# Optimization experiments

Measured on AMD Instinct MI355X. Metric: run time of the kernel, lower is better.

## Reference

```python
import jax, jax.numpy as jnp
import numpy as np
from jax import lax

L, D, H, V = 4, 128, 4, 33
d = D // H  # 32
B, T = 32, 4096

def rms(x, w, eps=1e-5):
    ms = jnp.mean(x.astype(jnp.float32) ** 2, axis=-1, keepdims=True)
    return (x * lax.rsqrt(ms + eps).astype(x.dtype)) * w

def l2n(x, eps=1e-6):
    return x * lax.rsqrt(jnp.sum(x * x, axis=-1, keepdims=True) + eps)

def causal_conv(h, w, b):
    # h: [B,T,D], w: [D,1,K] depthwise, b: [D]; causal via left-pad K-1
    K = w.shape[-1]
    y = lax.conv_general_dilated(h.transpose(0, 2, 1), w, (1,), [(K - 1, 0)],
                                 feature_group_count=h.shape[-1],
                                 dimension_numbers=('NCH', 'OIH', 'NCH'))
    return y.transpose(0, 2, 1) + b

def delta_scan(q, k, v, beta):
    # q,k,v: [B,T,H,d]; beta: [B,T,H]. Rank-1 delta-rule recurrence over T.
    xs = tuple(jnp.moveaxis(a, 1, 0) for a in (q, k, v, beta))
    S0 = jnp.zeros((q.shape[0], q.shape[2], q.shape[3], q.shape[3]), q.dtype)
    def step(S, inp):
        qt, kt, vt, bt = inp
        err = (vt - jnp.einsum('bhij,bhi->bhj', S, kt)) * bt[..., None]
        S = S + kt[..., :, None] * err[..., None, :]
        return S, jnp.einsum('bhij,bhi->bhj', S, qt)
    _, o = lax.scan(step, S0, xs)
    return jnp.moveaxis(o, 0, 1)  # [B,T,H,d]

def setup_inputs() -> dict:
    key = jax.random.key(0)
    ks = iter(jax.random.split(key, 40))
    def rn(shape, scale=0.02):
        return jax.random.normal(next(ks), shape, jnp.float32) * scale
    return {
        'x': jax.random.randint(next(ks), (B, T), 0, V),
        'emb': rn((V, D)),
        'qw': rn((L, D, D)), 'kw': rn((L, D, D)), 'vw': rn((L, D, D)),
        'qcw': rn((L, D, 1, 4), 0.2), 'qcb': rn((L, D)),
        'kcw': rn((L, D, 1, 4), 0.2), 'kcb': rn((L, D)),
        'vcw': rn((L, D, 1, 4), 0.2), 'vcb': rn((L, D)),
        'ow': rn((L, D, D)), 'gw': rn((L, D, D)), 'bw': rn((L, H, D)),
        'hnw': jnp.ones((L, d), jnp.float32),
        'n1w': jnp.ones((L, D), jnp.float32), 'n2w': jnp.ones((L, D), jnp.float32),
        'm1w': rn((L, 2 * D, D)), 'm2w': rn((L, D, 2 * D)),
        'fnw': jnp.ones((D,), jnp.float32), 'hw': rn((V, D)),
    }

def reference(x, emb, qw, kw, vw, qcw, qcb, kcw, kcb, vcw, vcb, ow, gw, bw,
              hnw, n1w, n2w, m1w, m2w, fnw, hw):
    silu = jax.nn.silu
    h = emb[x]  # [B,T,D]
    for l in range(L):
        hn = rms(h, n1w[l])
        q = l2n(silu(causal_conv(hn @ qw[l].T, qcw[l], qcb[l])).reshape(B, T, H, d)) / jnp.sqrt(jnp.float32(d))
        k = l2n(silu(causal_conv(hn @ kw[l].T, kcw[l], kcb[l])).reshape(B, T, H, d))
        v = silu(causal_conv(hn @ vw[l].T, vcw[l], vcb[l])).reshape(B, T, H, d)
        gate = (hn @ gw[l].T).reshape(B, T, H, d)
        beta = jax.nn.sigmoid(hn @ bw[l].T)  # [B,T,H]
        o = delta_scan(q, k, v, beta)
        o = rms(o, hnw[l]) * silu(gate)
        h = h + o.reshape(B, T, D) @ ow[l].T
        h = h + silu(rms(h, n2w[l]) @ m1w[l].T) @ m2w[l].T
    return rms(h, fnw) @ hw.T  # [B,T,V]
```

## Files before the change

kernel.cpp:

```cpp
#include <hip/hip_runtime.h>
#include <hip/hip_bf16.h>
#include <math.h>

#define BB 32
#define TT 4096
#define DD 128
#define HH 4
#define dh 32
#define VV 33
#define LL 4
#define MM (BB*TT)
#define NCHUNK (MM/128)
#define NC 64

typedef short short8 __attribute__((ext_vector_type(8)));
typedef float f32x4 __attribute__((ext_vector_type(4)));

__device__ __forceinline__ float b2f(unsigned short u){
  union{float f; unsigned int x;} v; v.x = ((unsigned int)u)<<16; return v.f;
}
__device__ __forceinline__ unsigned short f2b(float f){
  union{float f; unsigned int x;} v; v.f=f;
  unsigned int r = v.x + 0x7fffu + ((v.x>>16)&1u);
  return (unsigned short)(r>>16);
}
__device__ __forceinline__ float blo(unsigned int u){ union{float f;unsigned int x;}v; v.x=u<<16; return v.f;}
__device__ __forceinline__ float bhi(unsigned int u){ union{float f;unsigned int x;}v; v.x=u&0xffff0000u; return v.f;}
__device__ __forceinline__ float siluf(float x){ return x/(1.0f+expf(-x)); }

__global__ __launch_bounds__(256) void k_embed(const int* __restrict__ x, const float* __restrict__ emb,
                                               float* __restrict__ h){
  int i = blockIdx.x*256 + threadIdx.x;
  int bt = i>>7, c = i&127;
  h[i] = emb[x[bt]*DD + c];
}

__global__ __launch_bounds__(256) void k_rms(const float* __restrict__ src, const float* __restrict__ w,
                                             unsigned short* __restrict__ dst){
  int row = blockIdx.x*4 + (threadIdx.x>>6);
  int lane = threadIdx.x&63;
  const float2 xv = *(const float2*)(src + (size_t)row*DD + lane*2);
  float ss = xv.x*xv.x + xv.y*xv.y;
  #pragma unroll
  for (int m=1;m<64;m<<=1) ss += __shfl_xor(ss,m,64);
  float sc = rsqrtf(ss*(1.0f/128.0f)+1e-5f);
  const float2 wv = *(const float2*)(w + lane*2);
  unsigned int o = ((unsigned int)f2b(xv.y*sc*wv.y)<<16) | (unsigned int)f2b(xv.x*sc*wv.x);
  *(unsigned int*)(dst + (size_t)row*DD + lane*2) = o;
}

template<int NP, int ACT, int OUTADD>
__global__ __launch_bounds__(256) void k_gemm(const unsigned short* __restrict__ A,
                                              const float* __restrict__ W,
                                              void* __restrict__ outp, int N, int K){
  __shared__ __align__(16) unsigned short As[128*128];
  __shared__ __align__(16) unsigned short Ws[64*128];
  const int tid = threadIdx.x;
  const int lane = tid & 63, wave = tid >> 6;
  const int row0 = blockIdx.x*128, colbase = blockIdx.y*(64*NP);
  const int wr0 = (wave&1)*64, wc0 = (wave>>1)*32;
  const int fr = lane & 15, fq = lane >> 4;
  f32x4 acc[NP][4][2];
  #pragma unroll
  for (int p=0;p<NP;p++)
    #pragma unroll
    for (int m=0;m<4;m++)
      #pragma unroll
      for (int n=0;n<2;n++) acc[p][m][n] = (f32x4){0.f,0.f,0.f,0.f};

  for (int kc=0; kc<K; kc+=128){
    #pragma unroll
    for (int ii=0; ii<8; ++ii){
      int flat = tid + ii*256;
      int r = flat>>4, g = flat&15;
      uint4 gv = *(const uint4*)(A + (size_t)(row0+r)*K + kc + g*8);
      *(uint4*)&As[r*128 + ((g^(r&7))<<3)] = gv;
    }
    #pragma unroll
    for (int p=0;p<NP;p++){
      const int col0 = colbase + p*64;
      #pragma unroll
      for (int ii=0; ii<8; ++ii){
        int flat = tid + ii*256;
        int n = flat>>5, q4 = flat&31;
        float4 wv = *(const float4*)(W + (size_t)(col0+n)*K + kc + q4*4);
        uint2 pk;
        pk.x = (unsigned int)f2b(wv.x) | ((unsigned int)f2b(wv.y)<<16);
        pk.y = (unsigned int)f2b(wv.z) | ((unsigned int)f2b(wv.w)<<16);
        int dst = n*128 + ((((q4>>1)^(n&7))<<3) | ((q4&1)<<2));
        *(uint2*)&Ws[dst] = pk;
      }
      __syncthreads();
      #pragma unroll
      for (int ks=0; ks<4; ++ks){
        int gg = ks*4 + fq;
        short8 a[4], b[2];
        #pragma unroll
        for (int m=0;m<4;m++){
          int row = wr0 + m*16 + fr;
          a[m] = *(const short8*)&As[row*128 + ((gg^(row&7))<<3)];
        }
        #pragma unroll
        for (int n=0;n<2;n++){
          int col = wc0 + n*16 + fr;
          b[n] = *(const short8*)&Ws[col*128 + ((gg^(col&7))<<3)];
        }
        #pragma unroll
        for (int m=0;m<4;m++){
          #pragma unroll
          for (int n=0;n<2;n++)
            acc[p][m][n] = __builtin_amdgcn_mfma_f32_16x16x32_bf16(a[m], b[n], acc[p][m][n], 0, 0, 0);
        }
      }
      __syncthreads();
    }
  }

  #pragma unroll
  for (int p=0;p<NP;p++){
    const int col0 = colbase + p*64;
    if (OUTADD){
      float* O = (float*)outp;
      #pragma unroll
      for (int m=0;m<4;m++){
        #pragma unroll
        for (int n=0;n<2;n++){
          int ccol = col0 + wc0 + n*16 + fr;
          #pragma unroll
          for (int r=0;r<4;r++){
            int rrow = row0 + wr0 + m*16 + fq*4 + r;
            O[(size_t)rrow*N + ccol] += acc[p][m][n][r];
          }
        }
      }
    } else {
      unsigned short* O = (unsigned short*)outp;
      #pragma unroll
      for (int m=0;m<4;m++){
        #pragma unroll
        for (int n=0;n<2;n++){
          int ccol = col0 + wc0 + n*16 + fr;
          #pragma unroll
          for (int r=0;r<4;r++){
            int rrow = row0 + wr0 + m*16 + fq*4 + r;
            float vv = acc[p][m][n][r];
            if (ACT) vv = siluf(vv);
            O[(size_t)rrow*N + ccol] = f2b(vv);
          }
        }
      }
    }
  }
}

__global__ __launch_bounds__(256) void k_headm(const unsigned short* __restrict__ A,
                                               const float* __restrict__ W,
                                               float* __restrict__ out){
  __shared__ __align__(16) unsigned short As[128*128];
  __shared__ __align__(16) unsigned short Ws[64*128];
  const int tid = threadIdx.x;
  const int lane = tid & 63, wave = tid >> 6;
  const int row0 = blockIdx.x*128;
  const int wr0 = (wave&1)*64, wc0 = (wave>>1)*32;
  const int fr = lane & 15, fq = lane >> 4;
  f32x4 acc[4][2];
  #pragma unroll
  for (int m=0;m<4;m++)
    #pragma unroll
    for (int n=0;n<2;n++) acc[m][n] = (f32x4){0.f,0.f,0.f,0.f};

  #pragma unroll
  for (int ii=0; ii<8; ++ii){
    int flat = tid + ii*256;
    int r = flat>>4, g = flat&15;
    uint4 gv = *(const uint4*)(A + (size_t)(row0+r)*DD + g*8);
    *(uint4*)&As[r*128 + ((g^(r&7))<<3)] = gv;
  }
  #pragma unroll
  for (int ii=0; ii<8; ++ii){
    int flat = tid + ii*256;
    int n = flat>>5, q4 = flat&31;
    float4 wv = (n < VV) ? *(const float4*)(W + (size_t)n*DD + q4*4)
                         : (float4){0.f,0.f,0.f,0.f};
    uint2 pk;
    pk.x = (unsigned int)f2b(wv.x) | ((unsigned int)f2b(wv.y)<<16);
    pk.y = (unsigned int)f2b(wv.z) | ((unsigned int)f2b(wv.w)<<16);
    int dst = n*128 + ((((q4>>1)^(n&7))<<3) | ((q4&1)<<2));
    *(uint2*)&Ws[dst] = pk;
  }
  __syncthreads();
  #pragma unroll
  for (int ks=0; ks<4; ++ks){
    int gg = ks*4 + fq;
    short8 a[4], b[2];
    #pragma unroll
    for (int m=0;m<4;m++){
      int row = wr0 + m*16 + fr;
      a[m] = *(const short8*)&As[row*128 + ((gg^(row&7))<<3)];
    }
    #pragma unroll
    for (int n=0;n<2;n++){
      int col = wc0 + n*16 + fr;
      b[n] = *(const short8*)&Ws[col*128 + ((gg^(col&7))<<3)];
    }
    #pragma unroll
    for (int m=0;m<4;m++){
      #pragma unroll
      for (int n=0;n<2;n++)
        acc[m][n] = __builtin_amdgcn_mfma_f32_16x16x32_bf16(a[m], b[n], acc[m][n], 0, 0, 0);
    }
  }
  #pragma unroll
  for (int m=0;m<4;m++){
    #pragma unroll
    for (int n=0;n<2;n++){
      int ccol = wc0 + n*16 + fr;
      if (ccol < VV){
        #pragma unroll
        for (int r=0;r<4;r++){
          int rrow = row0 + wr0 + m*16 + fq*4 + r;
          out[(size_t)rrow*VV + ccol] = acc[m][n][r];
        }
      }
    }
  }
}

__global__ __launch_bounds__(256) void k_beta(const unsigned short* __restrict__ hn,
                                              const float* __restrict__ bwl, float* __restrict__ beta){
  __shared__ unsigned short As[64*128];
  int tid = threadIdx.x; int row0 = blockIdx.x*64;
  #pragma unroll
  for (int ii=0;ii<4;ii++){
    int flat = tid + ii*256;
    int r = flat>>4, v16 = flat&15;
    *(uint4*)&As[r*128 + v16*8] = *(const uint4*)(hn + (size_t)(row0+r)*DD + v16*8);
  }
  __syncthreads();
  int r = tid>>2, n = tid&3;
  const float* wr = bwl + n*DD;
  const unsigned short* ar = &As[r*128];
  float s = 0.f;
  #pragma unroll
  for (int k=0;k<128;k+=8){
    uint4 a = *(const uint4*)(ar + k);
    float4 wa = *(const float4*)(wr + k);
    float4 wb = *(const float4*)(wr + k + 4);
    s += blo(a.x)*wa.x + bhi(a.x)*wa.y + blo(a.y)*wa.z + bhi(a.y)*wa.w;
    s += blo(a.z)*wb.x + bhi(a.z)*wb.y + blo(a.w)*wb.z + bhi(a.w)*wb.w;
  }
  beta[(size_t)(row0+r)*HH + n] = 1.0f/(1.0f+expf(-s));
}

__global__ __launch_bounds__(256) void k_halo(const unsigned short* __restrict__ A,
                                              const unsigned short* __restrict__ B,
                                              const unsigned short* __restrict__ C,
                                              unsigned short* __restrict__ halo){
  int i = blockIdx.x*256 + threadIdx.x;
  int ch = i & 127;
  int rt = i >> 7;
  int r3 = rt % 3;
  int tn = (rt/3) % 3;
  int ck = rt / 9;
  unsigned short v = 0;
  if ((ck & 31) != 0){
    const unsigned short* X = (tn==0) ? A : (tn==1) ? B : C;
    v = X[((size_t)ck*128 - 3 + r3)*DD + ch];
  }
  halo[(size_t)i] = v;
}

__global__ __launch_bounds__(256) void k_conv_ip(
    unsigned short* __restrict__ A, unsigned short* __restrict__ B, unsigned short* __restrict__ C,
    const float* __restrict__ qcw, const float* __restrict__ qcb,
    const float* __restrict__ kcw, const float* __restrict__ kcb,
    const float* __restrict__ vcw, const float* __restrict__ vcb,
    const unsigned short* __restrict__ halo){
  __shared__ __align__(16) unsigned short Xs[131*128];
  const int tid = threadIdx.x;
  const int ck = blockIdx.x, tn = blockIdx.y;
  unsigned short* X = (tn==0) ? A : (tn==1) ? B : C;
  const float* w = (tn==0) ? qcw : (tn==1) ? kcw : vcw;
  const float* bi = (tn==0) ? qcb : (tn==1) ? kcb : vcb;

  if (tid < 48){
    int lr = tid>>4, c16 = tid&15;
    *(uint4*)&Xs[lr*128 + c16*8] = *(const uint4*)&halo[((size_t)(ck*3+tn)*3 + lr)*128 + c16*8];
  }
  #pragma unroll
  for (int ii=0; ii<8; ++ii){
    int flat = tid + ii*256;
    int r = flat>>4, c16 = flat&15;
    *(uint4*)&Xs[(3+r)*128 + c16*8] = *(const uint4*)&X[((size_t)ck*128 + r)*DD + c16*8];
  }
  __syncthreads();

  const int rh = tid>>7, c = tid&127;
  float w0=w[c*4+0], w1=w[c*4+1], w2=w[c*4+2], w3=w[c*4+3];
  float bc = bi[c];
  #pragma unroll 2
  for (int rr=0; rr<64; ++rr){
    int row = rr*2 + rh;
    float y = bc + w0*b2f(Xs[(row+0)*128+c]) + w1*b2f(Xs[(row+1)*128+c])
                 + w2*b2f(Xs[(row+2)*128+c]) + w3*b2f(Xs[(row+3)*128+c]);
    y = siluf(y);
    if (tn < 2){
      float s = y*y;
      #pragma unroll
      for (int m=1;m<32;m<<=1) s += __shfl_xor(s,m,64);
      y *= rsqrtf(s + 1e-6f);
      if (tn==0) y *= 0.17677669529663687f;
    }
    X[((size_t)ck*128 + row)*DD + c] = f2b(y);
  }
}

__global__ __launch_bounds__(256) void k_pA(const unsigned short* __restrict__ kbuf,
                                            unsigned short* vwbuf,
                                            const float* __restrict__ betab,
                                            unsigned short* __restrict__ Ubuf){
  __shared__ float Abt[64][68];
  __shared__ float sol[64][72];
  __shared__ float bs[64];
  const int c = blockIdx.x, bh = blockIdx.y;
  const int b = bh>>2, h = bh&3;
  const int tid = threadIdx.x;
  const int wave = tid>>6, lane = tid&63;
  const int fr = lane&15, fg = lane>>4;
  const size_t base = ((size_t)b*TT + c*64)*128 + h*32;
  const size_t bbase = ((size_t)b*TT + c*64)*4 + h;
  const size_t ub = ((size_t)bh*NC + c)*2048;

  if (tid < 64) bs[tid] = betab[bbase + (size_t)tid*4];

  short8 kA  = *(const short8*)(kbuf + base + (size_t)(wave*16+fr)*128 + fg*8);
  short8 kB0 = *(const short8*)(kbuf + base + (size_t)( 0+fr)*128 + fg*8);
  short8 kB1 = *(const short8*)(kbuf + base + (size_t)(16+fr)*128 + fg*8);
  short8 kB2 = *(const short8*)(kbuf + base + (size_t)(32+fr)*128 + fg*8);
  short8 kB3 = *(const short8*)(kbuf + base + (size_t)(48+fr)*128 + fg*8);
  __syncthreads();

  {
    float4 bsv = *(const float4*)&bs[wave*16 + fg*4];
    f32x4 a;
    #define BUILD(nt, kB) if (wave >= nt){ \
      a = (f32x4){0.f,0.f,0.f,0.f}; \
      a = __builtin_amdgcn_mfma_f32_16x16x32_bf16(kA, kB, a, 0,0,0); \
      Abt[nt*16+fr][wave*16+fg*4+0] = a[0]*bsv.x; \
      Abt[nt*16+fr][wave*16+fg*4+1] = a[1]*bsv.y; \
      Abt[nt*16+fr][wave*16+fg*4+2] = a[2]*bsv.z; \
      Abt[nt*16+fr][wave*16+fg*4+3] = a[3]*bsv.w; }
    BUILD(0, kB0) BUILD(1, kB1) BUILD(2, kB2) BUILD(3, kB3)
    #undef BUILD
  }

  const unsigned short* xp = ((lane<32)? (const unsigned short*)vwbuf : kbuf) + base + (lane&31);
  float racc[16];
  #pragma unroll
  for (int r=0;r<16;r++)
    racc[r] = b2f(xp[(size_t)(wave*16+r)*128]) * bs[wave*16+r];

  #pragma unroll
  for (int p=0;p<4;p++){
    if (wave == p){
      #pragma unroll
      for (int r=0;r<16;r++){
        float w_ = racc[r];
        sol[p*16+r][lane] = w_;
        #pragma unroll
        for (int r2=r+1;r2<16;r2++)
          racc[r2] -= Abt[p*16+r][p*16+r2] * w_;
      }
    }
    __syncthreads();
    if (wave > p){
      #pragma unroll
      for (int s16=0;s16<16;s16++){
        float w_ = sol[p*16+s16][lane];
        #pragma unroll
        for (int r=0;r<16;r++)
          racc[r] -= Abt[p*16+s16][wave*16+r] * w_;
      }
    }
    __syncthreads();
  }

  {
    int row = tid>>2, qt = tid&3;
    if (qt < 2){
      #pragma unroll
      for (int i=0;i<8;i++){
        int col = qt*16 + i*2;
        unsigned int pk = (unsigned int)f2b(sol[row][col]) | ((unsigned int)f2b(sol[row][col+1])<<16);
        *(unsigned int*)(vwbuf + base + (size_t)row*128 + col) = pk;
      }
    } else {
      #pragma unroll
      for (int i=0;i<8;i++){
        int col = (qt-2)*16 + i*2;
        unsigned int pk = (unsigned int)f2b(sol[row][32+col]) | ((unsigned int)f2b(sol[row][33+col])<<16);
        *(unsigned int*)(Ubuf + ub + row*32 + col) = pk;
      }
    }
  }
}

template<int PREC>
__global__ __launch_bounds__(64) void k_pB(const unsigned short* __restrict__ kbuf,
                                           unsigned short* webuf,
                                           const unsigned short* __restrict__ Ubuf,
                                           void* __restrict__ SentP){
  __shared__ float Sl[32][33];
  __shared__ unsigned short El[64][40];
  __shared__ unsigned short Ell[64][40];
  __shared__ unsigned short Kl[64][40];
  const int bh = blockIdx.x, b = bh>>2, h = bh&3;
  const int lane = threadIdx.x, fr = lane&15, fg = lane>>4;
  for (int i=lane; i<32*33; i+=64) ((float*)Sl)[i] = 0.f;
  f32x4 sc[2][2];
  #pragma unroll
  for (int it=0;it<2;it++){
    #pragma unroll
    for (int ct=0;ct<2;ct++) sc[it][ct]=(f32x4){0.f,0.f,0.f,0.f};
  }

  for (int c=0;c<NC;c++){
    const size_t base = ((size_t)b*TT + c*64)*128 + h*32;
    const size_t ub = ((size_t)bh*NC + c)*2048;
    {
      const unsigned short* kr = kbuf + base + (size_t)lane*128;
      const unsigned short* wr = webuf + base + (size_t)lane*128;
      uint4 a0=*(const uint4*)(kr),   a1=*(const uint4*)(kr+8);
      uint4 a2=*(const uint4*)(kr+16),a3=*(const uint4*)(kr+24);
      uint4 b0=*(const uint4*)(wr),   b1=*(const uint4*)(wr+8);
      uint4 b2=*(const uint4*)(wr+16),b3=*(const uint4*)(wr+24);
      *(uint4*)&Kl[lane][0]=a0; *(uint4*)&Kl[lane][8]=a1;
      *(uint4*)&Kl[lane][16]=a2; *(uint4*)&Kl[lane][24]=a3;
      *(uint4*)&El[lane][0]=b0; *(uint4*)&El[lane][8]=b1;
      *(uint4*)&El[lane][16]=b2; *(uint4*)&El[lane][24]=b3;
    }
    short8 uf[4];
    #pragma unroll
    for (int mt=0;mt<4;mt++)
      uf[mt] = *(const short8*)(Ubuf + ub + (size_t)(mt*16+fr)*32 + fg*8);
    f32x4 acc[4][2];
    #pragma unroll
    for (int mt=0;mt<4;mt++){
      #pragma unroll
      for (int ct=0;ct<2;ct++){
        #pragma unroll
        for (int r=0;r<4;r++)
          acc[mt][ct][r] = b2f(El[mt*16+fg*4+r][ct*16+fr]);
      }
    }
    short8 sb[2], sbl[2];
    #pragma unroll
    for (int ct=0;ct<2;ct++){
      short8 neg, negl;
      float pos[8];
      #pragma unroll
      for (int jj=0;jj<8;jj++){
        float sv = Sl[fg*8+jj][ct*16+fr];
        pos[jj] = sv;
        float nv = -sv;
        unsigned short hi = f2b(nv);
        neg[jj]=(short)hi;
        negl[jj]=(short)f2b(nv - b2f(hi));
      }
      sb[ct]=neg; sbl[ct]=negl;
      if (PREC){
        float* Sf = (float*)SentP + ((size_t)bh*NC + c)*1024 + ct*512 + lane*8;
        *(float4*)Sf     = (float4){pos[0],pos[1],pos[2],pos[3]};
        *(float4*)(Sf+4) = (float4){pos[4],pos[5],pos[6],pos[7]};
      } else {
        short8 p8;
        #pragma unroll
        for (int jj=0;jj<8;jj++) p8[jj]=(short)f2b(pos[jj]);
        *(short8*)((unsigned short*)SentP + ((size_t)bh*NC + c)*1024 + ct*512 + lane*8) = p8;
      }
    }
    #pragma unroll
    for (int mt=0;mt<4;mt++){
      #pragma unroll
      for (int ct=0;ct<2;ct++){
        acc[mt][ct] = __builtin_amdgcn_mfma_f32_16x16x32_bf16(uf[mt], sb[ct],  acc[mt][ct],0,0,0);
        acc[mt][ct] = __builtin_amdgcn_mfma_f32_16x16x32_bf16(uf[mt], sbl[ct], acc[mt][ct],0,0,0);
      }
    }
    #pragma unroll
    for (int mt=0;mt<4;mt++){
      #pragma unroll
      for (int ct=0;ct<2;ct++){
        #pragma unroll
        for (int r=0;r<4;r++){
          float ef = acc[mt][ct][r];
          unsigned short eh = f2b(ef);
          int t = mt*16+fg*4+r, j = ct*16+fr;
          El[t][j] = eh;
          Ell[t][j] = f2b(ef - b2f(eh));
          webuf[base + (size_t)t*128 + j] = eh;
        }
      }
    }
    short8 ka[2][2], eb[2][2], ebl[2][2];
    #pragma unroll
    for (int it=0;it<2;it++){
      #pragma unroll
      for (int ks=0;ks<2;ks++){
        short8 tmp;
        #pragma unroll
        for (int jj=0;jj<8;jj++) tmp[jj] = (short)Kl[ks*32+fg*8+jj][it*16+fr];
        ka[it][ks]=tmp;
      }
    }
    #pragma unroll
    for (int ct=0;ct<2;ct++){
      #pragma unroll
      for (int ks=0;ks<2;ks++){
        short8 t1v, t2v;
        #pragma unroll
        for (int jj=0;jj<8;jj++){
          t1v[jj] = (short)El[ks*32+fg*8+jj][ct*16+fr];
          t2v[jj] = (short)Ell[ks*32+fg*8+jj][ct*16+fr];
        }
        eb[ct][ks]=t1v; ebl[ct][ks]=t2v;
      }
    }
    #pragma unroll
    for (int it=0;it<2;it++){
      #pragma unroll
      for (int ct=0;ct<2;ct++){
        #pragma unroll
        for (int ks=0;ks<2;ks++){
          sc[it][ct] = __builtin_amdgcn_mfma_f32_16x16x32_bf16(ka[it][ks], eb[ct][ks],  sc[it][ct],0,0,0);
          sc[it][ct] = __builtin_amdgcn_mfma_f32_16x16x32_bf16(ka[it][ks], ebl[ct][ks], sc[it][ct],0,0,0);
        }
      }
    }
    #pragma unroll
    for (int it=0;it<2;it++){
      #pragma unroll
      for (int ct=0;ct<2;ct++){
        #pragma unroll
        for (int r=0;r<4;r++)
          Sl[it*16+fg*4+r][ct*16+fr] = sc[it][ct][r];
      }
    }
  }
}

template<int PREC>
__global__ __launch_bounds__(64) void k_pC(unsigned short* qobuf,
                                           const unsigned short* __restrict__ kbuf,
                                           const unsigned short* __restrict__ ebuf,
                                           const void* __restrict__ SentP){
  __shared__ unsigned short Pl[64][72];
  __shared__ unsigned short Plo[64][72];
  __shared__ unsigned short El[64][40];
  const int c = blockIdx.x, bh = blockIdx.y, b=bh>>2, h=bh&3;
  const int lane=threadIdx.x, fr=lane&15, fg=lane>>4;
  const size_t base = ((size_t)b*TT + c*64)*128 + h*32;
  #pragma unroll
  for (int i=0;i<9;i++){
    *(uint4*)&Pl[lane][i*8]  = (uint4){0u,0u,0u,0u};
    *(uint4*)&Plo[lane][i*8] = (uint4){0u,0u,0u,0u};
  }
  {
    const unsigned short* er = ebuf + base + (size_t)lane*128;
    uint4 a0=*(const uint4*)(er),   a1=*(const uint4*)(er+8);
    uint4 a2=*(const uint4*)(er+16),a3=*(const uint4*)(er+24);
    *(uint4*)&El[lane][0]=a0; *(uint4*)&El[lane][8]=a1;
    *(uint4*)&El[lane][16]=a2; *(uint4*)&El[lane][24]=a3;
  }
  short8 qf[4], kf[4];
  #pragma unroll
  for (int mt=0;mt<4;mt++){
    qf[mt] = *(const short8*)(qobuf + base + (size_t)(mt*16+fr)*128 + fg*8);
    kf[mt] = *(const short8*)(kbuf  + base + (size_t)(mt*16+fr)*128 + fg*8);
  }
  #pragma unroll
  for (int mt=0;mt<4;mt++){
    #pragma unroll
    for (int nt=0;nt<4;nt++){
      if (nt>mt) continue;
      f32x4 p = (f32x4){0.f,0.f,0.f,0.f};
      p = __builtin_amdgcn_mfma_f32_16x16x32_bf16(qf[mt], kf[nt], p,0,0,0);
      #pragma unroll
      for (int r=0;r<4;r++){
        int t = mt*16+fg*4+r, s = nt*16+fr;
        float pv = p[r];
        unsigned short ph = f2b(pv);
        Pl[t][s]  = (s<=t)? ph : (unsigned short)0;
        Plo[t][s] = (s<=t)? f2b(pv - b2f(ph)) : (unsigned short)0;
      }
    }
  }
  f32x4 acc[4][2];
  #pragma unroll
  for (int mt=0;mt<4;mt++){
    #pragma unroll
    for (int ct=0;ct<2;ct++) acc[mt][ct]=(f32x4){0.f,0.f,0.f,0.f};
  }
  if (PREC){
    short8 sfh[2], sfl[2];
    #pragma unroll
    for (int ct=0;ct<2;ct++){
      const float* Sf = (const float*)SentP + ((size_t)bh*NC + c)*1024 + ct*512 + lane*8;
      float4 v0 = *(const float4*)Sf;
      float4 v1 = *(const float4*)(Sf+4);
      float sv[8] = {v0.x,v0.y,v0.z,v0.w,v1.x,v1.y,v1.z,v1.w};
      short8 hh, ll;
      #pragma unroll
      for (int jj=0;jj<8;jj++){
        unsigned short hi = f2b(sv[jj]);
        hh[jj]=(short)hi; ll[jj]=(short)f2b(sv[jj]-b2f(hi));
      }
      sfh[ct]=hh; sfl[ct]=ll;
    }
    #pragma unroll
    for (int mt=0;mt<4;mt++){
      #pragma unroll
      for (int ct=0;ct<2;ct++){
        acc[mt][ct]=__builtin_amdgcn_mfma_f32_16x16x32_bf16(qf[mt], sfh[ct], acc[mt][ct],0,0,0);
        acc[mt][ct]=__builtin_amdgcn_mfma_f32_16x16x32_bf16(qf[mt], sfl[ct], acc[mt][ct],0,0,0);
      }
    }
  } else {
    short8 sf[2];
    #pragma unroll
    for (int ct=0;ct<2;ct++)
      sf[ct] = *(const short8*)((const unsigned short*)SentP + ((size_t)bh*NC + c)*1024 + ct*512 + lane*8);
    #pragma unroll
    for (int mt=0;mt<4;mt++){
      #pragma unroll
      for (int ct=0;ct<2;ct++)
        acc[mt][ct]=__builtin_amdgcn_mfma_f32_16x16x32_bf16(qf[mt], sf[ct], acc[mt][ct],0,0,0);
    }
  }
  short8 ebf[2][2];
  #pragma unroll
  for (int ct=0;ct<2;ct++){
    #pragma unroll
    for (int ks=0;ks<2;ks++){
      short8 tmp;
      #pragma unroll
      for (int jj=0;jj<8;jj++) tmp[jj]=(short)El[ks*32+fg*8+jj][ct*16+fr];
      ebf[ct][ks]=tmp;
    }
  }
  #pragma unroll
  for (int mt=0;mt<4;mt++){
    #pragma unroll
    for (int ks=0;ks<2;ks++){
      short8 pa  = *(const short8*)&Pl[mt*16+fr][ks*32+fg*8];
      short8 pal = *(const short8*)&Plo[mt*16+fr][ks*32+fg*8];
      #pragma unroll
      for (int ct=0;ct<2;ct++){
        acc[mt][ct]=__builtin_amdgcn_mfma_f32_16x16x32_bf16(pa,  ebf[ct][ks], acc[mt][ct],0,0,0);
        acc[mt][ct]=__builtin_amdgcn_mfma_f32_16x16x32_bf16(pal, ebf[ct][ks], acc[mt][ct],0,0,0);
      }
    }
  }
  #pragma unroll
  for (int mt=0;mt<4;mt++){
    #pragma unroll
    for (int ct=0;ct<2;ct++){
      #pragma unroll
      for (int r=0;r<4;r++)
        qobuf[base + (size_t)(mt*16+fg*4+r)*128 + ct*16+fr] = f2b(acc[mt][ct][r]);
    }
  }
}

__global__ __launch_bounds__(64) void k_scan(const unsigned short* q, const unsigned short* k,
                                             const unsigned short* v, const float* beta,
                                             unsigned short* o){
  int b = blockIdx.x>>2, hh = blockIdx.x&3;
  int lane = threadIdx.x;
  int j = lane&31, ih = lane>>5;
  float S[16];
  #pragma unroll
  for (int m=0;m<16;m++) S[m]=0.f;
  size_t idx0 = ((size_t)b*TT*HH + hh)*dh;
  size_t bidx0 = (size_t)b*TT*HH + hh;
  const unsigned short* kp = k + idx0 + ih*16;
  const unsigned short* qp = q + idx0 + ih*16;
  for (int t=0;t<TT;t++){
    size_t ofs=(size_t)t*128;
    uint4 ka=*(const uint4*)(kp+ofs), kb=*(const uint4*)(kp+ofs+8);
    uint4 qa=*(const uint4*)(qp+ofs), qb=*(const uint4*)(qp+ofs+8);
    float kf[16], qf[16];
    kf[0]=blo(ka.x);kf[1]=bhi(ka.x);kf[2]=blo(ka.y);kf[3]=bhi(ka.y);
    kf[4]=blo(ka.z);kf[5]=bhi(ka.z);kf[6]=blo(ka.w);kf[7]=bhi(ka.w);
    kf[8]=blo(kb.x);kf[9]=bhi(kb.x);kf[10]=blo(kb.y);kf[11]=bhi(kb.y);
    kf[12]=blo(kb.z);kf[13]=bhi(kb.z);kf[14]=blo(kb.w);kf[15]=bhi(kb.w);
    qf[0]=blo(qa.x);qf[1]=bhi(qa.x);qf[2]=blo(qa.y);qf[3]=bhi(qa.y);
    qf[4]=blo(qa.z);qf[5]=bhi(qa.z);qf[6]=blo(qa.w);qf[7]=bhi(qa.w);
    qf[8]=blo(qb.x);qf[9]=bhi(qb.x);qf[10]=blo(qb.y);qf[11]=bhi(qb.y);
    qf[12]=blo(qb.z);qf[13]=bhi(qb.z);qf[14]=blo(qb.w);qf[15]=bhi(qb.w);
    float vc = b2f(v[idx0+ofs+j]), bc = beta[bidx0+(size_t)t*4];
    float p0=0,p1=0,p2=0,p3=0;
    #pragma unroll
    for (int m=0;m<4;m++){
      p0 += S[m]*kf[m]; p1 += S[m+4]*kf[m+4]; p2 += S[m+8]*kf[m+8]; p3 += S[m+12]*kf[m+12];
    }
    float p = (p0+p1)+(p2+p3);
    p += __shfl_xor(p, 32, 64);
    float err = (vc - p)*bc;
    float o0=0,o1=0,o2=0,o3=0;
    #pragma unroll
    for (int m=0;m<4;m++){
      S[m]    += kf[m]*err;     o0 += S[m]*qf[m];
      S[m+4]  += kf[m+4]*err;   o1 += S[m+4]*qf[m+4];
      S[m+8]  += kf[m+8]*err;   o2 += S[m+8]*qf[m+8];
      S[m+12] += kf[m+12]*err;  o3 += S[m+12]*qf[m+12];
    }
    float oo = (o0+o1)+(o2+o3);
    oo += __shfl_xor(oo, 32, 64);
    if (ih==0) o[idx0 + ofs + j] = f2b(oo);
  }
}

__global__ __launch_bounds__(256) void k_ogate(const unsigned short* __restrict__ o, const unsigned short* __restrict__ gate,
                                               const float* __restrict__ hnwl, unsigned short* __restrict__ tmp){
  int tid=threadIdx.x;
  size_t bt = (size_t)blockIdx.x*2 + (tid>>7);
  int c = tid&127;
  size_t i = bt*DD + c;
  float ov = b2f(o[i]);
  float ss = ov*ov;
  #pragma unroll
  for (int m=1;m<32;m<<=1) ss += __shfl_xor(ss,m,64);
  float r = rsqrtf(ss*(1.0f/32.0f)+1e-5f);
  float g = b2f(gate[i]);
  tmp[i] = f2b(ov*r*hnwl[c&31]*siluf(g));
}

extern "C" void kernel_launch(void* const* d_in, const int* in_sizes, int n_in,
                              void* d_out, int out_size, void* d_ws, size_t ws_size,
                              hipStream_t stream){
  const int*   x   = (const int*)d_in[0];
  const float* emb = (const float*)d_in[1];
  const float* qw  = (const float*)d_in[2];
  const float* kw  = (const float*)d_in[3];
  const float* vw  = (const float*)d_in[4];
  const float* qcw = (const float*)d_in[5];
  const float* qcb = (const float*)d_in[6];
  const float* kcw = (const float*)d_in[7];
  const float* kcb = (const float*)d_in[8];
  const float* vcw = (const float*)d_in[9];
  const float* vcb = (const float*)d_in[10];
  const float* ow  = (const float*)d_in[11];
  const float* gw  = (const float*)d_in[12];
  const float* bw  = (const float*)d_in[13];
  const float* hnw = (const float*)d_in[14];
  const float* n1w = (const float*)d_in[15];
  const float* n2w = (const float*)d_in[16];
  const float* m1w = (const float*)d_in[17];
  const float* m2w = (const float*)d_in[18];
  const float* fnw = (const float*)d_in[19];
  const float* hw  = (const float*)d_in[20];

  char* ws = (char*)d_ws;
  size_t off = 0;
  float* h             = (float*)(ws+off);          off += (size_t)MM*DD*4;
  unsigned short* hn   = (unsigned short*)(ws+off); off += (size_t)MM*DD*2;
  unsigned short* A    = (unsigned short*)(ws+off); off += (size_t)MM*DD*2;
  unsigned short* B    = (unsigned short*)(ws+off); off += (size_t)MM*DD*2;
  unsigned short* C    = (unsigned short*)(ws+off); off += (size_t)MM*DD*2;
  float* beta          = (float*)(ws+off);          off += (size_t)MM*HH*4;
  unsigned short* halo = (unsigned short*)(ws+off); off += (size_t)NCHUNK*9*128*2;
  unsigned short* U    = (unsigned short*)(ws+off); off += (size_t)MM*DD*2;
  void* SentP          = (void*)(ws+off);
  const size_t NEED1 = off + (size_t)8192*1024*4;
  const size_t NEED0 = off + (size_t)8192*1024*2;
  unsigned short* t1   = A;
  const int mode = (ws_size >= NEED1) ? 1 : (ws_size >= NEED0) ? 0 : -1;

  k_embed<<<MM*DD/256, 256, 0, stream>>>(x, emb, h);
  for (int l=0;l<LL;l++){
    k_rms<<<MM/4,256,0,stream>>>(h, n1w + l*DD, hn);
    k_gemm<2,0,0><<<dim3(MM/128,1),256,0,stream>>>(hn, qw + l*DD*DD, A, 128, 128);
    k_gemm<2,0,0><<<dim3(MM/128,1),256,0,stream>>>(hn, kw + l*DD*DD, B, 128, 128);
    k_gemm<2,0,0><<<dim3(MM/128,1),256,0,stream>>>(hn, vw + l*DD*DD, C, 128, 128);
    k_beta<<<MM/64,256,0,stream>>>(hn, bw + l*HH*DD, beta);
    k_halo<<<NCHUNK*9*128/256,256,0,stream>>>(A, B, C, halo);
    k_conv_ip<<<dim3(NCHUNK,3),256,0,stream>>>(A, B, C,
                                  qcw+l*DD*4, qcb+l*DD, kcw+l*DD*4, kcb+l*DD, vcw+l*DD*4, vcb+l*DD,
                                  halo);
    if (mode >= 0){
      k_pA<<<dim3(NC, BB*HH), 256, 0, stream>>>(B, C, beta, U);
      if (mode==1){
        k_pB<1><<<BB*HH, 64, 0, stream>>>(B, C, U, SentP);
        k_pC<1><<<dim3(NC, BB*HH), 64, 0, stream>>>(A, B, C, SentP);
      } else {
        k_pB<0><<<BB*HH, 64, 0, stream>>>(B, C, U, SentP);
        k_pC<0><<<dim3(NC, BB*HH), 64, 0, stream>>>(A, B, C, SentP);
      }
    } else {
      k_scan<<<BB*HH,64,0,stream>>>(A, B, C, beta, A);
    }
    k_gemm<2,0,0><<<dim3(MM/128,1),256,0,stream>>>(hn, gw + l*DD*DD, C, 128, 128);
    k_ogate<<<MM/2,256,0,stream>>>(A, C, hnw+l*dh, B);
    k_gemm<2,0,1><<<dim3(MM/128,1),256,0,stream>>>(B, ow + l*DD*DD, h, 128, 128);
    k_rms<<<MM/4,256,0,stream>>>(h, n2w + l*DD, hn);
    k_gemm<2,1,0><<<dim3(MM/128,2),256,0,stream>>>(hn, m1w + l*2*DD*DD, t1, 256, 128);
    k_gemm<2,0,1><<<dim3(MM/128,1),256,0,stream>>>(t1, m2w + l*2*DD*DD, h, 128, 256);
  }
  k_rms<<<MM/4,256,0,stream>>>(h, fnw, hn);
  k_headm<<<MM/128,256,0,stream>>>(hn, hw, (float*)d_out);
}
```

Before: 2.831 ms.

## Fuse Q/K/V projections into one kernel and parallelize chunk-state scan over 4 waves

```diff
diff --git a/kernel.cpp b/kernel.cpp
--- a/kernel.cpp
+++ b/kernel.cpp
@@ -146,6 +146,88 @@
             float vv = acc[p][m][n][r];
             if (ACT) vv = siluf(vv);
             O[(size_t)rrow*N + ccol] = f2b(vv);
+          }
+        }
+      }
+    }
+  }
+}
+
+__global__ __launch_bounds__(256) void k_qkv(const unsigned short* __restrict__ Ain,
+                                             const float* __restrict__ qw,
+                                             const float* __restrict__ kw,
+                                             const float* __restrict__ vw,
+                                             unsigned short* __restrict__ Oq,
+                                             unsigned short* __restrict__ Ok,
+                                             unsigned short* __restrict__ Ov){
+  __shared__ __align__(16) unsigned short As[128*128];
+  __shared__ __align__(16) unsigned short Ws[64*128];
+  const int tid = threadIdx.x;
+  const int lane = tid & 63, wave = tid >> 6;
+  const int row0 = blockIdx.x*128;
+  const int wr0 = (wave&1)*64, wc0 = (wave>>1)*32;
+  const int fr = lane & 15, fq = lane >> 4;
+
+  #pragma unroll
+  for (int ii=0; ii<8; ++ii){
+    int flat = tid + ii*256;
+    int r = flat>>4, g = flat&15;
+    uint4 gv = *(const uint4*)(Ain + (size_t)(row0+r)*DD + g*8);
+    *(uint4*)&As[r*128 + ((g^(r&7))<<3)] = gv;
+  }
+  for (int t=0;t<3;t++){
+    const float* W = (t==0)?qw:(t==1)?kw:vw;
+    unsigned short* O = (t==0)?Oq:(t==1)?Ok:Ov;
+    for (int p=0;p<2;p++){
+      const int col0 = p*64;
+      #pragma unroll
+      for (int ii=0; ii<8; ++ii){
+        int flat = tid + ii*256;
+        int n = flat>>5, q4 = flat&31;
+        float4 wv = *(const float4*)(W + (size_t)(col0+n)*DD + q4*4);
+        uint2 pk;
+        pk.x = (unsigned int)f2b(wv.x) | ((unsigned int)f2b(wv.y)<<16);
+        pk.y = (unsigned int)f2b(wv.z) | ((unsigned int)f2b(wv.w)<<16);
+        int dst = n*128 + ((((q4>>1)^(n&7))<<3) | ((q4&1)<<2));
+        *(uint2*)&Ws[dst] = pk;
+      }
+      __syncthreads();
+      f32x4 acc[4][2];
+      #pragma unroll
+      for (int m=0;m<4;m++)
+        #pragma unroll
+        for (int n=0;n<2;n++) acc[m][n] = (f32x4){0.f,0.f,0.f,0.f};
+      #pragma unroll
+      for (int ks=0; ks<4; ++ks){
+        int gg = ks*4 + fq;
+        short8 a[4], b[2];
+        #pragma unroll
+        for (int m=0;m<4;m++){
+          int row = wr0 + m*16 + fr;
+          a[m] = *(const short8*)&As[row*128 + ((gg^(row&7))<<3)];
+        }
+        #pragma unroll
+        for (int n=0;n<2;n++){
+          int col = wc0 + n*16 + fr;
+          b[n] = *(const short8*)&Ws[col*128 + ((gg^(col&7))<<3)];
+        }
+        #pragma unroll
+        for (int m=0;m<4;m++){
+          #pragma unroll
+          for (int n=0;n<2;n++)
+            acc[m][n] = __builtin_amdgcn_mfma_f32_16x16x32_bf16(a[m], b[n], acc[m][n], 0, 0, 0);
+        }
+      }
+      __syncthreads();
+      #pragma unroll
+      for (int m=0;m<4;m++){
+        #pragma unroll
+        for (int n=0;n<2;n++){
+          int ccol = col0 + wc0 + n*16 + fr;
+          #pragma unroll
+          for (int r=0;r<4;r++){
+            int rrow = row0 + wr0 + m*16 + fq*4 + r;
+            O[(size_t)rrow*DD + ccol] = f2b(acc[m][n][r]);
           }
         }
       }
@@ -406,146 +488,109 @@
 }
 
 template<int PREC>
-__global__ __launch_bounds__(64) void k_pB(const unsigned short* __restrict__ kbuf,
+__global__ __launch_bounds__(256) void k_pB(const unsigned short* __restrict__ kbuf,
                                            unsigned short* webuf,
                                            const unsigned short* __restrict__ Ubuf,
                                            void* __restrict__ SentP){
   __shared__ float Sl[32][33];
+  __shared__ unsigned short Kl[64][40];
   __shared__ unsigned short El[64][40];
   __shared__ unsigned short Ell[64][40];
-  __shared__ unsigned short Kl[64][40];
   const int bh = blockIdx.x, b = bh>>2, h = bh&3;
-  const int lane = threadIdx.x, fr = lane&15, fg = lane>>4;
-  for (int i=lane; i<32*33; i+=64) ((float*)Sl)[i] = 0.f;
-  f32x4 sc[2][2];
-  #pragma unroll
-  for (int it=0;it<2;it++){
-    #pragma unroll
-    for (int ct=0;ct<2;ct++) sc[it][ct]=(f32x4){0.f,0.f,0.f,0.f};
-  }
+  const int tid = threadIdx.x, wave = tid>>6, lane = tid&63;
+  const int fr = lane&15, fg = lane>>4;
+  const int srow = tid>>2, sq = tid&3;
+  const int it = wave>>1, ctw = wave&1;
+  for (int i=tid; i<32*33; i+=256) ((float*)Sl)[i] = 0.f;
+  f32x4 sc = (f32x4){0.f,0.f,0.f,0.f};
+
+  const size_t base0 = ((size_t)b*TT)*128 + h*32;
+  const size_t ub0 = (size_t)bh*NC*2048;
+  uint4 pK = *(const uint4*)(kbuf  + base0 + (size_t)srow*128 + sq*8);
+  uint4 pW = *(const uint4*)(webuf + base0 + (size_t)srow*128 + sq*8);
+  uint4 pU = *(const uint4*)(Ubuf + ub0 + (size_t)(wave*16+fr)*32 + fg*8);
 
   for (int c=0;c<NC;c++){
-    const size_t base = ((size_t)b*TT + c*64)*128 + h*32;
-    const size_t ub = ((size_t)bh*NC + c)*2048;
-    {
-      const unsigned short* kr = kbuf + base + (size_t)lane*128;
-      const unsigned short* wr = webuf + base + (size_t)lane*128;
-      uint4 a0=*(const uint4*)(kr),   a1=*(const uint4*)(kr+8);
-      uint4 a2=*(const uint4*)(kr+16),a3=*(const uint4*)(kr+24);
-      uint4 b0=*(const uint4*)(wr),   b1=*(const uint4*)(wr+8);
-      uint4 b2=*(const uint4*)(wr+16),b3=*(const uint4*)(wr+24);
-      *(uint4*)&Kl[lane][0]=a0; *(uint4*)&Kl[lane][8]=a1;
-      *(uint4*)&Kl[lane][16]=a2; *(uint4*)&Kl[lane][24]=a3;
-      *(uint4*)&El[lane][0]=b0; *(uint4*)&El[lane][8]=b1;
-      *(uint4*)&El[lane][16]=b2; *(uint4*)&El[lane][24]=b3;
-    }
-    short8 uf[4];
-    #pragma unroll
-    for (int mt=0;mt<4;mt++)
-      uf[mt] = *(const short8*)(Ubuf + ub + (size_t)(mt*16+fr)*32 + fg*8);
-    f32x4 acc[4][2];
-    #pragma unroll
-    for (int mt=0;mt<4;mt++){
-      #pragma unroll
-      for (int ct=0;ct<2;ct++){
-        #pragma unroll
-        for (int r=0;r<4;r++)
-          acc[mt][ct][r] = b2f(El[mt*16+fg*4+r][ct*16+fr]);
-      }
+    const size_t cbase = ((size_t)b*TT + c*64)*128 + h*32;
+    __syncthreads();
+    *(uint4*)&Kl[srow][sq*8] = pK;
+    *(uint4*)&El[srow][sq*8] = pW;
+    short8 uf; { union{uint4 u; short8 s;} cv; cv.u = pU; uf = cv.s; }
+    __syncthreads();
+    if (c+1 < NC){
+      pK = *(const uint4*)(kbuf  + cbase + 64*128 + (size_t)srow*128 + sq*8);
+      pW = *(const uint4*)(webuf + cbase + 64*128 + (size_t)srow*128 + sq*8);
+      pU = *(const uint4*)(Ubuf + ub0 + (size_t)(c+1)*2048 + (size_t)(wave*16+fr)*32 + fg*8);
     }
     short8 sb[2], sbl[2];
     #pragma unroll
     for (int ct=0;ct<2;ct++){
-      short8 neg, negl;
-      float pos[8];
       #pragma unroll
       for (int jj=0;jj<8;jj++){
         float sv = Sl[fg*8+jj][ct*16+fr];
-        pos[jj] = sv;
         float nv = -sv;
         unsigned short hi = f2b(nv);
-        neg[jj]=(short)hi;
-        negl[jj]=(short)f2b(nv - b2f(hi));
-      }
-      sb[ct]=neg; sbl[ct]=negl;
+        sb[ct][jj] = (short)hi;
+        sbl[ct][jj] = (short)f2b(nv - b2f(hi));
+      }
+    }
+    if (wave==0){
       if (PREC){
-        float* Sf = (float*)SentP + ((size_t)bh*NC + c)*1024 + ct*512 + lane*8;
-        *(float4*)Sf     = (float4){pos[0],pos[1],pos[2],pos[3]};
-        *(float4*)(Sf+4) = (float4){pos[4],pos[5],pos[6],pos[7]};
+        #pragma unroll
+        for (int ct=0;ct<2;ct++){
+          float* Sf = (float*)SentP + ((size_t)bh*NC + c)*1024 + ct*512 + lane*8;
+          #pragma unroll
+          for (int jj=0;jj<8;jj++) Sf[jj] = Sl[fg*8+jj][ct*16+fr];
+        }
       } else {
-        short8 p8;
-        #pragma unroll
-        for (int jj=0;jj<8;jj++) p8[jj]=(short)f2b(pos[jj]);
-        *(short8*)((unsigned short*)SentP + ((size_t)bh*NC + c)*1024 + ct*512 + lane*8) = p8;
-      }
-    }
-    #pragma unroll
-    for (int mt=0;mt<4;mt++){
-      #pragma unroll
-      for (int ct=0;ct<2;ct++){
-        acc[mt][ct] = __builtin_amdgcn_mfma_f32_16x16x32_bf16(uf[mt], sb[ct],  acc[mt][ct],0,0,0);
-        acc[mt][ct] = __builtin_amdgcn_mfma_f32_16x16x32_bf16(uf[mt], sbl[ct], acc[mt][ct],0,0,0);
-      }
-    }
-    #pragma unroll
-    for (int mt=0;mt<4;mt++){
-      #pragma unroll
-      for (int ct=0;ct<2;ct++){
-        #pragma unroll
-        for (int r=0;r<4;r++){
-          float ef = acc[mt][ct][r];
-          unsigned short eh = f2b(ef);
-          int t = mt*16+fg*4+r, j = ct*16+fr;
-          El[t][j] = eh;
-          Ell[t][j] = f2b(ef - b2f(eh));
-          webuf[base + (size_t)t*128 + j] = eh;
-        }
-      }
-    }
-    short8 ka[2][2], eb[2][2], ebl[2][2];
-    #pragma unroll
-    for (int it=0;it<2;it++){
-      #pragma unroll
-      for (int ks=0;ks<2;ks++){
-        short8 tmp;
-        #pragma unroll
-        for (int jj=0;jj<8;jj++) tmp[jj] = (short)Kl[ks*32+fg*8+jj][it*16+fr];
-        ka[it][ks]=tmp;
-      }
-    }
+        #pragma unroll
+        for (int ct=0;ct<2;ct++){
+          unsigned short* Sf = (unsigned short*)SentP + ((size_t)bh*NC + c)*1024 + ct*512 + lane*8;
+          #pragma unroll
+          for (int jj=0;jj<8;jj++) Sf[jj] = f2b(Sl[fg*8+jj][ct*16+fr]);
+        }
+      }
+    }
+    f32x4 acc[2];
     #pragma unroll
     for (int ct=0;ct<2;ct++){
       #pragma unroll
-      for (int ks=0;ks<2;ks++){
-        short8 t1v, t2v;
-        #pragma unroll
-        for (int jj=0;jj<8;jj++){
-          t1v[jj] = (short)El[ks*32+fg*8+jj][ct*16+fr];
-          t2v[jj] = (short)Ell[ks*32+fg*8+jj][ct*16+fr];
-        }
-        eb[ct][ks]=t1v; ebl[ct][ks]=t2v;
-      }
-    }
-    #pragma unroll
-    for (int it=0;it<2;it++){
-      #pragma unroll
-      for (int ct=0;ct<2;ct++){
-        #pragma unroll
-        for (int ks=0;ks<2;ks++){
-          sc[it][ct] = __builtin_amdgcn_mfma_f32_16x16x32_bf16(ka[it][ks], eb[ct][ks],  sc[it][ct],0,0,0);
-          sc[it][ct] = __builtin_amdgcn_mfma_f32_16x16x32_bf16(ka[it][ks], ebl[ct][ks], sc[it][ct],0,0,0);
-        }
-      }
-    }
-    #pragma unroll
-    for (int it=0;it<2;it++){
-      #pragma unroll
-      for (int ct=0;ct<2;ct++){
-        #pragma unroll
-        for (int r=0;r<4;r++)
-          Sl[it*16+fg*4+r][ct*16+fr] = sc[it][ct][r];
-      }
-    }
+      for (int r=0;r<4;r++)
+        acc[ct][r] = b2f(El[wave*16+fg*4+r][ct*16+fr]);
+    }
+    #pragma unroll
+    for (int ct=0;ct<2;ct++){
+      acc[ct] = __builtin_amdgcn_mfma_f32_16x16x32_bf16(uf, sb[ct],  acc[ct],0,0,0);
+      acc[ct] = __builtin_amdgcn_mfma_f32_16x16x32_bf16(uf, sbl[ct], acc[ct],0,0,0);
+    }
+    #pragma unroll
+    for (int ct=0;ct<2;ct++){
+      #pragma unroll
+      for (int r=0;r<4;r++){
+        float ef = acc[ct][r];
+        unsigned short eh = f2b(ef);
+        int t = wave*16+fg*4+r, j = ct*16+fr;
+        El[t][j] = eh;
+        Ell[t][j] = f2b(ef - b2f(eh));
+        webuf[cbase + (size_t)t*128 + j] = eh;
+      }
+    }
+    __syncthreads();
+    #pragma unroll
+    for (int ks=0;ks<2;ks++){
+      short8 ka, eb, ebl;
+      #pragma unroll
+      for (int jj=0;jj<8;jj++){
+        ka[jj]  = (short)Kl [ks*32+fg*8+jj][it*16+fr];
+        eb[jj]  = (short)El [ks*32+fg*8+jj][ctw*16+fr];
+        ebl[jj] = (short)Ell[ks*32+fg*8+jj][ctw*16+fr];
+      }
+      sc = __builtin_amdgcn_mfma_f32_16x16x32_bf16(ka, eb,  sc,0,0,0);
+      sc = __builtin_amdgcn_mfma_f32_16x16x32_bf16(ka, ebl, sc,0,0,0);
+    }
+    #pragma unroll
+    for (int r=0;r<4;r++)
+      Sl[it*16+fg*4+r][ctw*16+fr] = sc[r];
   }
 }
 
@@ -780,9 +825,7 @@
   k_embed<<<MM*DD/256, 256, 0, stream>>>(x, emb, h);
   for (int l=0;l<LL;l++){
     k_rms<<<MM/4,256,0,stream>>>(h, n1w + l*DD, hn);
-    k_gemm<2,0,0><<<dim3(MM/128,1),256,0,stream>>>(hn, qw + l*DD*DD, A, 128, 128);
-    k_gemm<2,0,0><<<dim3(MM/128,1),256,0,stream>>>(hn, kw + l*DD*DD, B, 128, 128);
-    k_gemm<2,0,0><<<dim3(MM/128,1),256,0,stream>>>(hn, vw + l*DD*DD, C, 128, 128);
+    k_qkv<<<MM/128,256,0,stream>>>(hn, qw + l*DD*DD, kw + l*DD*DD, vw + l*DD*DD, A, B, C);
     k_beta<<<MM/64,256,0,stream>>>(hn, bw + l*HH*DD, beta);
     k_halo<<<NCHUNK*9*128/256,256,0,stream>>>(A, B, C, halo);
     k_conv_ip<<<dim3(NCHUNK,3),256,0,stream>>>(A, B, C,
@@ -791,10 +834,10 @@
     if (mode >= 0){
       k_pA<<<dim3(NC, BB*HH), 256, 0, stream>>>(B, C, beta, U);
       if (mode==1){
-        k_pB<1><<<BB*HH, 64, 0, stream>>>(B, C, U, SentP);
+        k_pB<1><<<BB*HH, 256, 0, stream>>>(B, C, U, SentP);
         k_pC<1><<<dim3(NC, BB*HH), 64, 0, stream>>>(A, B, C, SentP);
       } else {
-        k_pB<0><<<BB*HH, 64, 0, stream>>>(B, C, U, SentP);
+        k_pB<0><<<BB*HH, 256, 0, stream>>>(B, C, U, SentP);
         k_pC<0><<<dim3(NC, BB*HH), 64, 0, stream>>>(A, B, C, SentP);
       }
     } else {
```

Result: faster. 2.717 ms (-4.0%).
